# Kernel tuning notes

Measured on AMD Instinct MI355X. Metric: run time of the kernel, lower is better.

The kernel has to match this reference:

```python
import jax, jax.numpy as jnp
import numpy as np

B, S, D, H = 2, 2048, 1024, 16
DH = D // H  # dim_per_head = 64


def setup_inputs() -> dict:
    key = jax.random.key(0)
    ks = jax.random.split(key, 12)
    std = 1.0 / np.sqrt(D)
    inp = {
        "key": jax.random.normal(ks[0], (B, S, D), jnp.float32),
        "value": jax.random.normal(ks[1], (B, S, D), jnp.float32),
        "query": jax.random.normal(ks[2], (B, S, D), jnp.float32),
        "mask": jax.random.randint(ks[3], (B, S, S), 0, 2) == 1,
        "Wk": jax.random.normal(ks[4], (D, D), jnp.float32) * std,
        "bk": jnp.zeros((D,), jnp.float32),
        "Wv": jax.random.normal(ks[5], (D, D), jnp.float32) * std,
        "bv": jnp.zeros((D,), jnp.float32),
        "Wq": jax.random.normal(ks[6], (D, D), jnp.float32) * std,
        "bq": jnp.zeros((D,), jnp.float32),
        "Wo": jax.random.normal(ks[7], (D, D), jnp.float32) * std,
        "bo": jnp.zeros((D,), jnp.float32),
    }
    return inp


def _shape(x):
    # (B, L, D) -> (B, H, L, DH)
    return x.reshape(B, -1, H, DH).transpose(0, 2, 1, 3)


def reference(key, value, query, mask, Wk, bk, Wv, bv, Wq, bq, Wo, bo):
    k = _shape(key @ Wk.T + bk)      # (B,H,S,DH)
    v = _shape(value @ Wv.T + bv)    # (B,H,S,DH)
    q = _shape(query @ Wq.T + bq)    # (B,H,S,DH)
    q = q / jnp.sqrt(jnp.asarray(DH, q.dtype))
    scores = jnp.einsum("bhqd,bhkd->bhqk", q, k).astype(jnp.float32)
    scores = jnp.where(mask[:, None, :, :], jnp.float32(-1e18), scores)
    attn = jax.nn.softmax(scores, axis=-1).astype(q.dtype)  # (B,H,S,S)
    # dropout p=0.0 -> identity
    ctx = jnp.einsum("bhqk,bhkd->bhqd", attn, v)
    ctx = ctx.transpose(0, 2, 1, 3).reshape(B, -1, D)
    output = ctx @ Wo.T + bo
    top_attn = attn[:, 0, :, :]
    return output, top_attn
```

## Files before the change

### kernel.cpp

```cpp
#include <hip/hip_runtime.h>

constexpr int BB = 2, SS = 2048, DD = 1024, HH = 16, DHH = 64;

typedef __attribute__((ext_vector_type(4))) float f32x4;
typedef __attribute__((ext_vector_type(8))) __bf16 bf16x8;
typedef __attribute__((ext_vector_type(8))) unsigned short us8;

__device__ __forceinline__ unsigned short f32_to_bf16(float f) {
    unsigned int u = __float_as_uint(f);
    u += 0x7fffu + ((u >> 16) & 1u);
    return (unsigned short)(u >> 16);
}

__device__ __forceinline__ ushort2 pk_bf16(float a, float b) {
#if __has_builtin(__builtin_amdgcn_cvt_pk_bf16_f32)
    typedef __attribute__((ext_vector_type(2))) __bf16 bf16x2;
    bf16x2 r = __builtin_amdgcn_cvt_pk_bf16_f32(a, b);
    return *(ushort2*)&r;
#else
    ushort2 r; r.x = f32_to_bf16(a); r.y = f32_to_bf16(b); return r;
#endif
}
__device__ __forceinline__ ushort4 pk_bf16x4(float a, float b, float c, float d) {
    const ushort2 lo = pk_bf16(a, b), hi = pk_bf16(c, d);
    ushort4 r; r.x = lo.x; r.y = lo.y; r.z = hi.x; r.w = hi.y;
    return r;
}

__device__ __forceinline__ f32x4 mfma_bf16(bf16x8 a, bf16x8 b, f32x4 c) {
    return __builtin_amdgcn_mfma_f32_16x16x32_bf16(a, b, c, 0, 0, 0);
}

__device__ __forceinline__ void stage16(const void* g, void* l) {
    typedef const __attribute__((address_space(1))) unsigned int gas_t;
    typedef __attribute__((address_space(3))) unsigned int las_t;
    __builtin_amdgcn_global_load_lds((gas_t*)(unsigned long long)g,
                                     (las_t*)(unsigned int)(unsigned long long)l,
                                     16, 0, 0);
}

__global__ __launch_bounds__(256) void cvt_bf16(const float* __restrict__ src,
                                                unsigned short* __restrict__ dst) {
    const size_t i = ((size_t)blockIdx.x * 256 + threadIdx.x) * 8;
    const float4 a = *(const float4*)(src + i);
    const float4 b = *(const float4*)(src + i + 4);
    ushort4 lo = pk_bf16x4(a.x, a.y, a.z, a.w);
    ushort4 hi = pk_bf16x4(b.x, b.y, b.z, b.w);
    us8 o;
    o[0] = lo.x; o[1] = lo.y; o[2] = lo.z; o[3] = lo.w;
    o[4] = hi.x; o[5] = hi.y; o[6] = hi.z; o[7] = hi.w;
    *(us8*)(dst + i) = o;
}

__global__ __launch_bounds__(256) void mask_pack(const int* __restrict__ mask,
                                                 unsigned long long* __restrict__ pm) {
    const int t = threadIdx.x;
    const size_t chunk = (size_t)blockIdx.x * 4 + (t >> 6);
    const int lane = t & 63;
    const int v = mask[chunk * 64 + lane];
    const unsigned long long b = __ballot(v != 0);
    if (lane == 0) pm[chunk] = b;
}

template <int MODE>
__global__ __launch_bounds__(256) void gemm_nt(const unsigned short* __restrict__ A,
                                               const unsigned short* __restrict__ Wb,
                                               const float* __restrict__ bias,
                                               void* __restrict__ outp,
                                               float scale) {
    constexpr int K = DD;
    __shared__ __align__(16) unsigned short Ash[2][128][64];
    __shared__ __align__(16) unsigned short Bsh[2][64][64];

    const int m0 = blockIdx.x * 128;
    const int n0 = blockIdx.y * 64;
    const int t = threadIdx.x;
    const int lane = t & 63, w = t >> 6;
    const int l15 = lane & 15, quad = lane >> 4;
    const int wm = (w >> 1) * 64, wn = (w & 1) * 32;

    const int srow = lane >> 3;
    const int scol8 = ((lane & 7) ^ srow) * 8;
    const unsigned short* Ag = A + (size_t)(m0 + w * 32 + srow) * K + scol8;
    const unsigned short* Bg = Wb + (size_t)(n0 + w * 16 + srow) * K + scol8;

    f32x4 acc[4][2] = {};

#pragma unroll
    for (int j = 0; j < 4; ++j) stage16(Ag + (size_t)j * 8 * K, &Ash[0][w * 32 + j * 8][0]);
#pragma unroll
    for (int j = 0; j < 2; ++j) stage16(Bg + (size_t)j * 8 * K, &Bsh[0][w * 16 + j * 8][0]);

    for (int kk = 0; kk < K / 64; ++kk) {
        const int cur = kk & 1;
        if (kk < K / 64 - 1) {
            const size_t ko = (size_t)(kk + 1) * 64;
#pragma unroll
            for (int j = 0; j < 4; ++j)
                stage16(Ag + (size_t)j * 8 * K + ko, &Ash[cur ^ 1][w * 32 + j * 8][0]);
#pragma unroll
            for (int j = 0; j < 2; ++j)
                stage16(Bg + (size_t)j * 8 * K + ko, &Bsh[cur ^ 1][w * 16 + j * 8][0]);
            __asm__ volatile("s_waitcnt vmcnt(6)" ::: "memory");
        } else {
            __asm__ volatile("s_waitcnt vmcnt(0)" ::: "memory");
        }
        __builtin_amdgcn_s_barrier();
        __builtin_amdgcn_sched_barrier(0);

        const unsigned short* Ab = &Ash[cur][0][0];
        const unsigned short* Bb = &Bsh[cur][0][0];

#pragma unroll
        for (int s = 0; s < 2; ++s) {
            const int ch = ((s * 4 + quad) ^ (l15 & 7)) * 8;
            bf16x8 af[4], bfr[2];
#pragma unroll
            for (int mi = 0; mi < 4; ++mi)
                af[mi] = *(const bf16x8*)&Ab[(wm + mi * 16 + l15) * 64 + ch];
#pragma unroll
            for (int ni = 0; ni < 2; ++ni)
                bfr[ni] = *(const bf16x8*)&Bb[(wn + ni * 16 + l15) * 64 + ch];
            __builtin_amdgcn_s_setprio(1);
#pragma unroll
            for (int mi = 0; mi < 4; ++mi)
#pragma unroll
                for (int ni = 0; ni < 2; ++ni)
                    acc[mi][ni] = mfma_bf16(af[mi], bfr[ni], acc[mi][ni]);
            __builtin_amdgcn_s_setprio(0);
        }
        __builtin_amdgcn_sched_barrier(0);
        __builtin_amdgcn_s_barrier();
        __builtin_amdgcn_sched_barrier(0);
    }

#pragma unroll
    for (int ni = 0; ni < 2; ++ni) {
        const int c = n0 + wn + ni * 16 + l15;
        const float bs = bias[c];
#pragma unroll
        for (int mi = 0; mi < 4; ++mi) {
#pragma unroll
            for (int r = 0; r < 4; ++r) {
                const int mrow = m0 + wm + mi * 16 + quad * 4 + r;
                const float val = (acc[mi][ni][r] + bs) * scale;
                if (MODE == 2) {
                    ((float*)outp)[(size_t)mrow * DD + c] = val;
                } else {
                    const int bi2 = mrow >> 11, si = mrow & (SS - 1);
                    const int hi2 = c >> 6, di = c & (DHH - 1);
                    unsigned short* o = (unsigned short*)outp;
                    if (MODE == 0)
                        o[((size_t)(bi2 * HH + hi2) * SS + si) * DHH + di] = f32_to_bf16(val);
                    else
                        o[((size_t)(bi2 * HH + hi2) * DHH + di) * SS + si] = f32_to_bf16(val);
                }
            }
        }
    }
}

__global__ __launch_bounds__(512, 4) void flash_attn(const unsigned short* __restrict__ qws,
                                                     const unsigned short* __restrict__ kws,
                                                     const unsigned short* __restrict__ vws,
                                                     const unsigned long long* __restrict__ pm,
                                                     unsigned short* __restrict__ ctx) {
    __shared__ __align__(16) unsigned short Ksh[2][64][64];
    __shared__ __align__(16) unsigned short Vsh[2][64][64];
    __shared__ __align__(16) unsigned short Psh[8][16][72];

    constexpr int NQT = SS / 128;
    const int qt = blockIdx.x % NQT;
    const int bh = blockIdx.x / NQT;
    const int bi = bh / HH, hi = bh % HH;

    const int t = threadIdx.x;
    const int lane = t & 63, w = t >> 6;
    const int l15 = lane & 15, quad = lane >> 4;
    const int sh4 = quad * 4;
    const int xk = quad ^ (l15 & 7);

    const unsigned short* qp = qws + (size_t)bh * SS * DHH;
    const unsigned short* kp = kws + (size_t)bh * SS * DHH;
    const unsigned short* vp = vws + (size_t)bh * DHH * SS;

    const int q_loc = qt * 128 + w * 16 + l15;
    const bf16x8 bq0 = *(const bf16x8*)(qp + (size_t)q_loc * DHH + quad * 8);
    const bf16x8 bq1 = *(const bf16x8*)(qp + (size_t)q_loc * DHH + 32 + quad * 8);
    const unsigned long long* pmrow = pm + ((size_t)bi * SS + q_loc) * (SS / 64);

    const int srow = lane >> 3;
    const int scol = (lane & 7) ^ srow;
    const unsigned short* kg = kp + (size_t)(w * 8 + srow) * DHH + scol * 8;
    const unsigned short* vg = vp + (size_t)(w * 8 + srow) * SS + scol * 8;

    f32x4 accO[4] = {};
    float m_run = -1e30f, l_run = 0.f;
    const float NEG_INF = -__builtin_inff();

    unsigned long long mcur = pmrow[0];
    stage16(kg, &Ksh[0][w * 8][0]);
    stage16(vg, &Vsh[0][w * 8][0]);

    constexpr int NT = SS / 64;
    for (int kt = 0; kt < NT; ++kt) {
        const int cur = kt & 1;
        unsigned long long mnxt = 0;
        if (kt < NT - 1) {
            mnxt = pmrow[kt + 1];
            stage16(kg + (size_t)(kt + 1) * 64 * DHH, &Ksh[cur ^ 1][w * 8][0]);
            stage16(vg + (size_t)(kt + 1) * 64,       &Vsh[cur ^ 1][w * 8][0]);
            __asm__ volatile("s_waitcnt vmcnt(3)" ::: "memory");
        } else {
            __asm__ volatile("s_waitcnt vmcnt(0)" ::: "memory");
        }
        __builtin_amdgcn_s_barrier();
        __builtin_amdgcn_sched_barrier(0);

        const unsigned short* Kb = &Ksh[cur][0][0];
        const unsigned short* Vb = &Vsh[cur][0][0];

        bf16x8 ak0[4], ak1[4];
#pragma unroll
        for (int i = 0; i < 4; ++i) {
            ak0[i] = *(const bf16x8*)&Kb[(i * 16 + l15) * 64 + xk * 8];
            ak1[i] = *(const bf16x8*)&Kb[(i * 16 + l15) * 64 + (xk ^ 4) * 8];
        }

        const unsigned int mlo = ((unsigned int)mcur) >> sh4;
        const unsigned int mhi = ((unsigned int)(mcur >> 32)) >> sh4;

        float sc[4][4];
        __builtin_amdgcn_s_setprio(1);
#pragma unroll
        for (int i = 0; i < 4; ++i) {
            f32x4 s4 = {};
            s4 = mfma_bf16(ak0[i], bq0, s4);
            s4 = mfma_bf16(ak1[i], bq1, s4);
            const unsigned int mw = (i & 2) ? mhi : mlo;
#pragma unroll
            for (int r = 0; r < 4; ++r)
                sc[i][r] = ((mw >> ((i & 1) * 16 + r)) & 1u) ? NEG_INF : s4[r];
        }
        __builtin_amdgcn_s_setprio(0);

        bf16x8 av0[4], av1[4];
#pragma unroll
        for (int i = 0; i < 4; ++i) {
            av0[i] = *(const bf16x8*)&Vb[(i * 16 + l15) * 64 + xk * 8];
            av1[i] = *(const bf16x8*)&Vb[(i * 16 + l15) * 64 + (xk ^ 4) * 8];
        }

        float tm = sc[0][0];
#pragma unroll
        for (int i = 0; i < 4; ++i)
#pragma unroll
            for (int r = 0; r < 4; ++r) tm = fmaxf(tm, sc[i][r]);
        tm = fmaxf(tm, __shfl_xor(tm, 16));
        tm = fmaxf(tm, __shfl_xor(tm, 32));

        const bool nodefer = !__all(tm <= m_run + 8.0f);
        const float mn = nodefer ? fmaxf(m_run, tm) : m_run;

        float rs = 0.f;
#pragma unroll
        for (int i = 0; i < 4; ++i)
#pragma unroll
            for (int r = 0; r < 4; ++r) {
                const float p = __builtin_amdgcn_exp2f(sc[i][r] - mn);
                sc[i][r] = p;
                rs += p;
            }
        rs += __shfl_xor(rs, 16);
        rs += __shfl_xor(rs, 32);

        if (nodefer) {
            const float alpha = __builtin_amdgcn_exp2f(m_run - mn);
            l_run = l_run * alpha + rs;
            m_run = mn;
#pragma unroll
            for (int i = 0; i < 4; ++i) accO[i] *= alpha;
        } else {
            l_run += rs;
        }

#pragma unroll
        for (int i = 0; i < 4; ++i)
            *(ushort4*)&Psh[w][l15][i * 16 + sh4] =
                pk_bf16x4(sc[i][0], sc[i][1], sc[i][2], sc[i][3]);
        __asm__ volatile("s_waitcnt lgkmcnt(0)" ::: "memory");

        const bf16x8 p0 = *(const bf16x8*)&Psh[w][l15][quad * 8];
        const bf16x8 p1 = *(const bf16x8*)&Psh[w][l15][32 + quad * 8];
        __builtin_amdgcn_s_setprio(1);
#pragma unroll
        for (int i = 0; i < 4; ++i) {
            accO[i] = mfma_bf16(av0[i], p0, accO[i]);
            accO[i] = mfma_bf16(av1[i], p1, accO[i]);
        }
        __builtin_amdgcn_s_setprio(0);

        __builtin_amdgcn_sched_barrier(0);
        __builtin_amdgcn_s_barrier();
        __builtin_amdgcn_sched_barrier(0);
        mcur = mnxt;
    }

    const float inv = 1.0f / l_run;
    unsigned short* cb = ctx + ((size_t)(bi * SS) + q_loc) * DD + hi * DHH;
#pragma unroll
    for (int i = 0; i < 4; ++i)
        *(ushort4*)&cb[i * 16 + sh4] = pk_bf16x4(accO[i][0] * inv, accO[i][1] * inv,
                                                 accO[i][2] * inv, accO[i][3] * inv);
}

__global__ __launch_bounds__(256) void score_h0(const unsigned short* __restrict__ q0,
                                                const unsigned short* __restrict__ k0,
                                                const unsigned long long* __restrict__ pm,
                                                float* __restrict__ outp,
                                                float2* __restrict__ stats) {
    __shared__ __align__(16) unsigned short Ksh[64][72];

    const int kc = blockIdx.x & 3;
    const int qt = (blockIdx.x >> 2) & 31;
    const int bi = blockIdx.x >> 7;

    const int t = threadIdx.x;
    const int lane = t & 63, w = t >> 6;
    const int l15 = lane & 15, quad = lane >> 4;
    const int sh4 = quad * 4;

    const int q = qt * 64 + w * 16 + l15;
    const unsigned short* qp = q0 + ((size_t)bi * SS + q) * DHH;
    const bf16x8 bq0 = *(const bf16x8*)(qp + quad * 8);
    const bf16x8 bq1 = *(const bf16x8*)(qp + 32 + quad * 8);

    const unsigned short* kp = k0 + (size_t)bi * SS * DHH;
    const unsigned long long* pmq = pm + ((size_t)bi * SS + q) * (SS / 64);
    float* orow = outp + ((size_t)bi * SS + q) * SS;

    float m_l = -1e30f, l_l = 0.f;

    for (int kt = 0; kt < 8; ++kt) {
        const int key0 = kc * 512 + kt * 64;
        __syncthreads();
#pragma unroll
        for (int hf = 0; hf < 2; ++hf) {
            const int v = t + hf * 256;
            const int row = v >> 3, off = (v & 7) * 8;
            *(us8*)&Ksh[row][off] = *(const us8*)(kp + (size_t)(key0 + row) * DHH + off);
        }
        __syncthreads();

        const unsigned long long m64 = pmq[kc * 8 + kt];
        const unsigned int mlo = ((unsigned int)m64) >> sh4;
        const unsigned int mhi = ((unsigned int)(m64 >> 32)) >> sh4;

        float sc[4][4];
        float lm = -1e30f;
#pragma unroll
        for (int i = 0; i < 4; ++i) {
            const bf16x8 ak0 = *(const bf16x8*)&Ksh[i * 16 + l15][quad * 8];
            const bf16x8 ak1 = *(const bf16x8*)&Ksh[i * 16 + l15][32 + quad * 8];
            f32x4 s4 = {};
            s4 = mfma_bf16(ak0, bq0, s4);
            s4 = mfma_bf16(ak1, bq1, s4);
            const unsigned int mw = (i & 2) ? mhi : mlo;
            float4 ov;
#pragma unroll
            for (int r = 0; r < 4; ++r) {
                const float s = ((mw >> ((i & 1) * 16 + r)) & 1u) ? -1e18f : s4[r];
                sc[i][r] = s;
                lm = fmaxf(lm, s);
            }
            ov.x = sc[i][0]; ov.y = sc[i][1]; ov.z = sc[i][2]; ov.w = sc[i][3];
            *(float4*)&orow[key0 + i * 16 + sh4] = ov;
        }

        const float mn = fmaxf(m_l, lm);
        float rs = 0.f;
#pragma unroll
        for (int i = 0; i < 4; ++i)
#pragma unroll
            for (int r = 0; r < 4; ++r) rs += __builtin_amdgcn_exp2f(sc[i][r] - mn);
        l_l = l_l * __builtin_amdgcn_exp2f(m_l - mn) + rs;
        m_l = mn;
    }

#pragma unroll
    for (int d = 16; d <= 32; d <<= 1) {
        const float mo = __shfl_xor(m_l, d);
        const float lo = __shfl_xor(l_l, d);
        const float mn = fmaxf(m_l, mo);
        l_l = l_l * __builtin_amdgcn_exp2f(m_l - mn) + lo * __builtin_amdgcn_exp2f(mo - mn);
        m_l = mn;
    }
    if (quad == 0) {
        float2 st; st.x = m_l; st.y = l_l;
        stats[((size_t)(bi * 4 + kc)) * SS + q] = st;
    }
}

__global__ __launch_bounds__(256) void scale_h0(float* __restrict__ scores,
                                                const float2* __restrict__ stats) {
    const int bi = blockIdx.x >> 11;
    const int si = blockIdx.x & (SS - 1);
    const int t = threadIdx.x;

    float M = -1e30f, L = 0.f;
#pragma unroll
    for (int c = 0; c < 4; ++c) {
        const float2 st = stats[((size_t)(bi * 4 + c)) * SS + si];
        const float mn = fmaxf(M, st.x);
        L = L * __builtin_amdgcn_exp2f(M - mn) + st.y * __builtin_amdgcn_exp2f(st.x - mn);
        M = mn;
    }
    const float inv = 1.0f / L;

    float* row = scores + (size_t)blockIdx.x * SS;
    const int base = t * 8;
    float4 a = *(const float4*)&row[base];
    float4 b = *(const float4*)&row[base + 4];
    a.x = __builtin_amdgcn_exp2f(a.x - M) * inv;
    a.y = __builtin_amdgcn_exp2f(a.y - M) * inv;
    a.z = __builtin_amdgcn_exp2f(a.z - M) * inv;
    a.w = __builtin_amdgcn_exp2f(a.w - M) * inv;
    b.x = __builtin_amdgcn_exp2f(b.x - M) * inv;
    b.y = __builtin_amdgcn_exp2f(b.y - M) * inv;
    b.z = __builtin_amdgcn_exp2f(b.z - M) * inv;
    b.w = __builtin_amdgcn_exp2f(b.w - M) * inv;
    *(float4*)&row[base] = a;
    *(float4*)&row[base + 4] = b;
}

extern "C" void kernel_launch(void* const* d_in, const int* in_sizes, int n_in,
                              void* d_out, int out_size, void* d_ws, size_t ws_size,
                              hipStream_t stream) {
    const float* key_   = (const float*)d_in[0];
    const float* value_ = (const float*)d_in[1];
    const float* query_ = (const float*)d_in[2];
    const int*   mask_  = (const int*)d_in[3];
    const float* Wk = (const float*)d_in[4];
    const float* bk = (const float*)d_in[5];
    const float* Wv = (const float*)d_in[6];
    const float* bv = (const float*)d_in[7];
    const float* Wq = (const float*)d_in[8];
    const float* bq = (const float*)d_in[9];
    const float* Wo = (const float*)d_in[10];
    const float* bo = (const float*)d_in[11];

    constexpr size_t XS  = (size_t)BB * SS * DD;
    constexpr size_t WSZ = (size_t)DD * DD;

    float* out_f = (float*)d_out;
    unsigned short* scratch = (unsigned short*)(out_f + XS);
    unsigned short* qws = scratch;
    unsigned short* kws = qws + XS;
    unsigned short* vws = kws + XS;
    unsigned short* ctx = vws + XS;

    unsigned short* q0 = (unsigned short*)d_ws;
    unsigned short* k0 = q0 + (size_t)BB * SS * DHH;
    unsigned long long* pm = (unsigned long long*)(k0 + (size_t)BB * SS * DHH);
    float2* stats = (float2*)(pm + (size_t)BB * SS * (SS / 64));

    unsigned short* Xq  = (unsigned short*)out_f;
    unsigned short* Xk  = Xq + XS;
    unsigned short* Xv  = kws;
    unsigned short* Wqb = ctx;
    unsigned short* Wkb = Wqb + WSZ;
    unsigned short* Wvb = Wkb + WSZ;
    unsigned short* Wob = qws;

    mask_pack<<<BB * SS * (SS / 64) / 4, 256, 0, stream>>>(mask_, pm);

    cvt_bf16<<<XS / 2048, 256, 0, stream>>>(query_, Xq);
    cvt_bf16<<<XS / 2048, 256, 0, stream>>>(key_,   Xk);
    cvt_bf16<<<XS / 2048, 256, 0, stream>>>(value_, Xv);
    cvt_bf16<<<WSZ / 2048, 256, 0, stream>>>(Wq, Wqb);
    cvt_bf16<<<WSZ / 2048, 256, 0, stream>>>(Wk, Wkb);
    cvt_bf16<<<WSZ / 2048, 256, 0, stream>>>(Wv, Wvb);

    const float qscale = 0.125f * 1.4426950408889634f;

    dim3 gg(BB * SS / 128, DD / 64);
    gemm_nt<0><<<gg, 256, 0, stream>>>(Xq, Wqb, bq, qws, qscale);
    gemm_nt<1><<<gg, 256, 0, stream>>>(Xv, Wvb, bv, vws, 1.0f);
    gemm_nt<0><<<gg, 256, 0, stream>>>(Xk, Wkb, bk, kws, 1.0f);

    for (int b = 0; b < BB; ++b) {
        hipMemcpyAsync(q0 + (size_t)b * SS * DHH, qws + (size_t)(b * HH) * SS * DHH,
                       (size_t)SS * DHH * sizeof(unsigned short),
                       hipMemcpyDeviceToDevice, stream);
        hipMemcpyAsync(k0 + (size_t)b * SS * DHH, kws + (size_t)(b * HH) * SS * DHH,
                       (size_t)SS * DHH * sizeof(unsigned short),
                       hipMemcpyDeviceToDevice, stream);
    }

    flash_attn<<<BB * HH * (SS / 128), 512, 0, stream>>>(qws, kws, vws, pm, ctx);

    cvt_bf16<<<WSZ / 2048, 256, 0, stream>>>(Wo, Wob);
    gemm_nt<2><<<gg, 256, 0, stream>>>(ctx, Wob, bo, out_f, 1.0f);

    score_h0<<<BB * 32 * 4, 256, 0, stream>>>(q0, k0, pm, out_f + XS, stats);
    scale_h0<<<BB * SS, 256, 0, stream>>>(out_f + XS, stats);
}
```

Measured before the change: 343.4 us.

## Reuse flash-attention softmax stats for head-0 probabilities and remap block IDs per XCD

Flash attention now writes the running max and sum for head 0, so the head-0 probability kernel can emit normalized probabilities in one pass. This removes the separate scale pass that re-read and rewrote the full BxSxS fp32 matrix, along with the partial-stat merge. Both GEMM and attention grids are also remapped so consecutive block IDs are spread across the 8 XCDs in groups, aiming for better L2 locality. One risk is that head-0 probabilities now depend on flash-attention stats computed from the same bf16 q/k, which should match.

```diff
diff --git a/kernel.cpp b/kernel.cpp
--- a/kernel.cpp
+++ b/kernel.cpp
@@ -72,8 +72,11 @@
     __shared__ __align__(16) unsigned short Ash[2][128][64];
     __shared__ __align__(16) unsigned short Bsh[2][64][64];
 
-    const int m0 = blockIdx.x * 128;
-    const int n0 = blockIdx.y * 64;
+    const int id = blockIdx.x;
+    const int nid = (id & 7) * 64 + (id >> 3);
+    const int n0 = (nid & 15) * 64;
+    const int m0 = (nid >> 4) * 128;
+
     const int t = threadIdx.x;
     const int lane = t & 63, w = t >> 6;
     const int l15 = lane & 15, quad = lane >> 4;
@@ -164,14 +167,17 @@
                                                      const unsigned short* __restrict__ kws,
                                                      const unsigned short* __restrict__ vws,
                                                      const unsigned long long* __restrict__ pm,
-                                                     unsigned short* __restrict__ ctx) {
+                                                     unsigned short* __restrict__ ctx,
+                                                     float2* __restrict__ stats) {
     __shared__ __align__(16) unsigned short Ksh[2][64][64];
     __shared__ __align__(16) unsigned short Vsh[2][64][64];
     __shared__ __align__(16) unsigned short Psh[8][16][72];
 
     constexpr int NQT = SS / 128;
-    const int qt = blockIdx.x % NQT;
-    const int bh = blockIdx.x / NQT;
+    const int id = blockIdx.x;
+    const int nid = (id & 7) * 64 + (id >> 3);
+    const int qt = nid % NQT;
+    const int bh = nid / NQT;
     const int bi = bh / HH, hi = bh % HH;
 
     const int t = threadIdx.x;
@@ -312,13 +318,18 @@
     for (int i = 0; i < 4; ++i)
         *(ushort4*)&cb[i * 16 + sh4] = pk_bf16x4(accO[i][0] * inv, accO[i][1] * inv,
                                                  accO[i][2] * inv, accO[i][3] * inv);
-}
-
-__global__ __launch_bounds__(256) void score_h0(const unsigned short* __restrict__ q0,
-                                                const unsigned short* __restrict__ k0,
-                                                const unsigned long long* __restrict__ pm,
-                                                float* __restrict__ outp,
-                                                float2* __restrict__ stats) {
+
+    if (hi == 0 && quad == 0) {
+        float2 st; st.x = m_run; st.y = l_run;
+        stats[(size_t)bi * SS + q_loc] = st;
+    }
+}
+
+__global__ __launch_bounds__(256) void prob_h0(const unsigned short* __restrict__ q0,
+                                               const unsigned short* __restrict__ k0,
+                                               const unsigned long long* __restrict__ pm,
+                                               const float2* __restrict__ stats,
+                                               float* __restrict__ outp) {
     __shared__ __align__(16) unsigned short Ksh[64][72];
 
     const int kc = blockIdx.x & 3;
@@ -339,7 +350,9 @@
     const unsigned long long* pmq = pm + ((size_t)bi * SS + q) * (SS / 64);
     float* orow = outp + ((size_t)bi * SS + q) * SS;
 
-    float m_l = -1e30f, l_l = 0.f;
+    const float2 st = stats[(size_t)bi * SS + q];
+    const float M = st.x;
+    const float invL = 1.0f / st.y;
 
     for (int kt = 0; kt < 8; ++kt) {
         const int key0 = kc * 512 + kt * 64;
@@ -356,8 +369,6 @@
         const unsigned int mlo = ((unsigned int)m64) >> sh4;
         const unsigned int mhi = ((unsigned int)(m64 >> 32)) >> sh4;
 
-        float sc[4][4];
-        float lm = -1e30f;
 #pragma unroll
         for (int i = 0; i < 4; ++i) {
             const bf16x8 ak0 = *(const bf16x8*)&Ksh[i * 16 + l15][quad * 8];
@@ -369,68 +380,12 @@
             float4 ov;
 #pragma unroll
             for (int r = 0; r < 4; ++r) {
-                const float s = ((mw >> ((i & 1) * 16 + r)) & 1u) ? -1e18f : s4[r];
-                sc[i][r] = s;
-                lm = fmaxf(lm, s);
+                const float p = __builtin_amdgcn_exp2f(s4[r] - M) * invL;
+                ((float*)&ov)[r] = ((mw >> ((i & 1) * 16 + r)) & 1u) ? 0.0f : p;
             }
-            ov.x = sc[i][0]; ov.y = sc[i][1]; ov.z = sc[i][2]; ov.w = sc[i][3];
             *(float4*)&orow[key0 + i * 16 + sh4] = ov;
         }
-
-        const float mn = fmaxf(m_l, lm);
-        float rs = 0.f;
-#pragma unroll
-        for (int i = 0; i < 4; ++i)
-#pragma unroll
-            for (int r = 0; r < 4; ++r) rs += __builtin_amdgcn_exp2f(sc[i][r] - mn);
-        l_l = l_l * __builtin_amdgcn_exp2f(m_l - mn) + rs;
-        m_l = mn;
-    }
-
-#pragma unroll
-    for (int d = 16; d <= 32; d <<= 1) {
-        const float mo = __shfl_xor(m_l, d);
-        const float lo = __shfl_xor(l_l, d);
-        const float mn = fmaxf(m_l, mo);
-        l_l = l_l * __builtin_amdgcn_exp2f(m_l - mn) + lo * __builtin_amdgcn_exp2f(mo - mn);
-        m_l = mn;
-    }
-    if (quad == 0) {
-        float2 st; st.x = m_l; st.y = l_l;
-        stats[((size_t)(bi * 4 + kc)) * SS + q] = st;
-    }
-}
-
-__global__ __launch_bounds__(256) void scale_h0(float* __restrict__ scores,
-                                                const float2* __restrict__ stats) {
-    const int bi = blockIdx.x >> 11;
-    const int si = blockIdx.x & (SS - 1);
-    const int t = threadIdx.x;
-
-    float M = -1e30f, L = 0.f;
-#pragma unroll
-    for (int c = 0; c < 4; ++c) {
-        const float2 st = stats[((size_t)(bi * 4 + c)) * SS + si];
-        const float mn = fmaxf(M, st.x);
-        L = L * __builtin_amdgcn_exp2f(M - mn) + st.y * __builtin_amdgcn_exp2f(st.x - mn);
-        M = mn;
-    }
-    const float inv = 1.0f / L;
-
-    float* row = scores + (size_t)blockIdx.x * SS;
-    const int base = t * 8;
-    float4 a = *(const float4*)&row[base];
-    float4 b = *(const float4*)&row[base + 4];
-    a.x = __builtin_amdgcn_exp2f(a.x - M) * inv;
-    a.y = __builtin_amdgcn_exp2f(a.y - M) * inv;
-    a.z = __builtin_amdgcn_exp2f(a.z - M) * inv;
-    a.w = __builtin_amdgcn_exp2f(a.w - M) * inv;
-    b.x = __builtin_amdgcn_exp2f(b.x - M) * inv;
-    b.y = __builtin_amdgcn_exp2f(b.y - M) * inv;
-    b.z = __builtin_amdgcn_exp2f(b.z - M) * inv;
-    b.w = __builtin_amdgcn_exp2f(b.w - M) * inv;
-    *(float4*)&row[base] = a;
-    *(float4*)&row[base + 4] = b;
+    }
 }
 
 extern "C" void kernel_launch(void* const* d_in, const int* in_sizes, int n_in,
@@ -483,10 +438,9 @@
 
     const float qscale = 0.125f * 1.4426950408889634f;
 
-    dim3 gg(BB * SS / 128, DD / 64);
-    gemm_nt<0><<<gg, 256, 0, stream>>>(Xq, Wqb, bq, qws, qscale);
-    gemm_nt<1><<<gg, 256, 0, stream>>>(Xv, Wvb, bv, vws, 1.0f);
-    gemm_nt<0><<<gg, 256, 0, stream>>>(Xk, Wkb, bk, kws, 1.0f);
+    gemm_nt<0><<<512, 256, 0, stream>>>(Xq, Wqb, bq, qws, qscale);
+    gemm_nt<1><<<512, 256, 0, stream>>>(Xv, Wvb, bv, vws, 1.0f);
+    gemm_nt<0><<<512, 256, 0, stream>>>(Xk, Wkb, bk, kws, 1.0f);
 
     for (int b = 0; b < BB; ++b) {
         hipMemcpyAsync(q0 + (size_t)b * SS * DHH, qws + (size_t)(b * HH) * SS * DHH,
@@ -497,11 +451,10 @@
                        hipMemcpyDeviceToDevice, stream);
     }
 
-    flash_attn<<<BB * HH * (SS / 128), 512, 0, stream>>>(qws, kws, vws, pm, ctx);
+    flash_attn<<<BB * HH * (SS / 128), 512, 0, stream>>>(qws, kws, vws, pm, ctx, stats);
 
     cvt_bf16<<<WSZ / 2048, 256, 0, stream>>>(Wo, Wob);
-    gemm_nt<2><<<gg, 256, 0, stream>>>(ctx, Wob, bo, out_f, 1.0f);
-
-    score_h0<<<BB * 32 * 4, 256, 0, stream>>>(q0, k0, pm, out_f + XS, stats);
-    scale_h0<<<BB * SS, 256, 0, stream>>>(out_f + XS, stats);
-}
+    gemm_nt<2><<<512, 256, 0, stream>>>(ctx, Wob, bo, out_f, 1.0f);
+
+    prob_h0<<<BB * 32 * 4, 256, 0, stream>>>(q0, k0, pm, stats, out_f + XS);
+}
```

Result: faster. 318.3 us (-7.3%).
